# Kernel tuning notes

Measured on AMD Instinct MI355X. Metric: run time of the kernel, lower is better.

## Reference

```python
import jax, jax.numpy as jnp
import numpy as np
import math

N = 8192
H = 128
W = 128
TILE = 16
FOVX = math.pi / 3.0
FOVY = math.pi / 3.0
FOCAL_X = W / (2.0 * math.tan(FOVX * 0.5))
FOCAL_Y = H / (2.0 * math.tan(FOVY * 0.5))
WHITE_BKGD = True

# spherical-harmonic constants (degree 0..3), standard 3DGS eval_sh
C0 = 0.28209479177387814
C1 = 0.4886025119029199
C2 = (1.0925484305920792, -1.0925484305920792, 0.31539156525252005,
      -1.0925484305920792, 0.5462742152960396)
C3 = (-0.5900435899266435, 2.890611442640554, -0.4570457994644658,
      0.3731763325901154, -0.4570457994644658, 1.445305721320277,
      -0.5900435899266435)


def eval_sh3(sh, dirs):
    # sh: [N,3,16], dirs: [N,3] (unnormalized, as in the source)
    x, y, z = dirs[:, 0:1], dirs[:, 1:2], dirs[:, 2:3]
    res = C0 * sh[..., 0]
    res = res - C1 * y * sh[..., 1] + C1 * z * sh[..., 2] - C1 * x * sh[..., 3]
    xx, yy, zz = x * x, y * y, z * z
    xy, yz, xz = x * y, y * z, x * z
    res = (res + C2[0] * xy * sh[..., 4] + C2[1] * yz * sh[..., 5]
           + C2[2] * (2 * zz - xx - yy) * sh[..., 6]
           + C2[3] * xz * sh[..., 7] + C2[4] * (xx - yy) * sh[..., 8])
    res = (res + C3[0] * y * (3 * xx - yy) * sh[..., 9]
           + C3[1] * xy * z * sh[..., 10]
           + C3[2] * y * (4 * zz - xx - yy) * sh[..., 11]
           + C3[3] * z * (2 * zz - 3 * xx - 3 * yy) * sh[..., 12]
           + C3[4] * x * (4 * zz - xx - yy) * sh[..., 13]
           + C3[5] * z * (xx - yy) * sh[..., 14]
           + C3[6] * x * (xx - 3 * yy) * sh[..., 15])
    return res  # [N,3]


def _forward(means3D, opacity, scales, rotations, shs, viewmatrix, projmatrix, camera_center):
    f32 = means3D.dtype
    # ---- projection_ndc (row-vector convention) ----
    pts_o = jnp.concatenate([means3D, jnp.ones_like(means3D[:, :1])], -1)  # [N,4]
    pts_h = pts_o @ viewmatrix @ projmatrix
    p_proj = pts_h / (pts_h[:, -1:] + 1e-6)
    p_view = pts_o @ viewmatrix
    depths = p_view[:, 2]  # all points pass in_mask (z>=0.2) by construction

    # ---- build_color: SH degree 3 ----
    rays_d = means3D - camera_center
    color = jnp.maximum(eval_sh3(jnp.swapaxes(shs, 1, 2), rays_d) + 0.5, 0.0)  # [N,3]

    # ---- build_covariance_3d: L = R(q) @ diag(s); cov3d = L L^T ----
    q = rotations / jnp.linalg.norm(rotations, axis=1, keepdims=True)
    r, x, y, z = q[:, 0], q[:, 1], q[:, 2], q[:, 3]
    R = jnp.stack([1 - 2 * (y * y + z * z), 2 * (x * y - r * z), 2 * (x * z + r * y),
                   2 * (x * y + r * z), 1 - 2 * (x * x + z * z), 2 * (y * z - r * x),
                   2 * (x * z - r * y), 2 * (y * z + r * x), 1 - 2 * (x * x + y * y)],
                  axis=1).reshape(-1, 3, 3)
    L = R * scales[:, None, :]  # right-multiply by diag(s)
    cov3d = jnp.einsum('nij,nkj->nik', L, L)

    # ---- build_covariance_2d ----
    tanx, tany = math.tan(FOVX * 0.5), math.tan(FOVY * 0.5)
    t = means3D @ viewmatrix[:3, :3] + viewmatrix[3:4, :3]
    tz = t[:, 2]
    tx = jnp.clip(t[:, 0] / tz, -1.3 * tanx, 1.3 * tanx) * tz
    ty = jnp.clip(t[:, 1] / tz, -1.3 * tany, 1.3 * tany) * tz
    zr = jnp.zeros_like(tz)
    J = jnp.stack([FOCAL_X / tz, zr, -tx * FOCAL_X / (tz * tz),
                   zr, FOCAL_Y / tz, -ty * FOCAL_Y / (tz * tz),
                   zr, zr, zr], axis=1).reshape(-1, 3, 3)
    Wm = viewmatrix[:3, :3].T
    M = jnp.einsum('ij,njk,lk->nil', Wm, cov3d, Wm)
    cov2d = jnp.einsum('nab,nbc,ndc->nad', J, M, J)[:, :2, :2] + 0.3 * jnp.eye(2, dtype=f32)

    means2D = jnp.stack([((p_proj[:, 0] + 1) * W - 1.0) * 0.5,
                         ((p_proj[:, 1] + 1) * H - 1.0) * 0.5], -1)  # [N,2]

    # ---- radii / rect (computed under no_grad in the source) ----
    c2 = jax.lax.stop_gradient(cov2d)
    m2_ng = jax.lax.stop_gradient(means2D)
    det_ng = c2[:, 0, 0] * c2[:, 1, 1] - c2[:, 0, 1] * c2[:, 1, 0]
    mid = 0.5 * (c2[:, 0, 0] + c2[:, 1, 1])
    sq = jnp.sqrt(jnp.maximum(mid * mid - det_ng, 0.1))
    lam1 = mid + sq
    lam2 = mid - sq
    radii = 3.0 * jnp.ceil(jnp.sqrt(jnp.maximum(lam1, lam2)))
    rmin = m2_ng - radii[:, None]
    rmax = m2_ng + radii[:, None]
    rmin = jnp.stack([jnp.clip(rmin[:, 0], 0.0, W - 1.0), jnp.clip(rmin[:, 1], 0.0, H - 1.0)], -1)
    rmax = jnp.stack([jnp.clip(rmax[:, 0], 0.0, W - 1.0), jnp.clip(rmax[:, 1], 0.0, H - 1.0)], -1)

    # ---- global front-to-back depth sort (per-tile sort of a depth-sorted
    # subset equals the global sort restricted to that subset) ----
    order = jnp.argsort(depths)
    m2d_s = means2D[order]
    cov_s = cov2d[order]
    dep_s = depths[order]
    op_s = opacity[order, 0]  # [N]
    col_s = color[order]
    rmin_s = rmin[order]
    rmax_s = rmax[order]

    # analytic 2x2 inverse (conic)
    a, b = cov_s[:, 0, 0], cov_s[:, 0, 1]
    c, d = cov_s[:, 1, 0], cov_s[:, 1, 1]
    idet = 1.0 / (a * d - b * c)
    c00, c11 = d * idet, a * idet
    c01, c10 = -b * idet, -c * idet
    cxy = c01 + c10

    ty_n, tx_n = H // TILE, W // TILE

    def render_tile(tid):
        h = (tid // tx_n) * TILE
        w = (tid % tx_n) * TILE
        px = w + jnp.arange(TILE)
        py = h + jnp.arange(TILE)
        gx, gy = jnp.meshgrid(px, py)  # 'xy': gx[i,j]=px[j], gy[i,j]=py[i]
        coord = jnp.stack([gx, gy], -1).reshape(-1, 2).astype(f32)  # [P,2]=(x,y)
        # tile overlap test (replaces the data-dependent boolean gather)
        tlx = jnp.maximum(rmin_s[:, 0], w)
        tly = jnp.maximum(rmin_s[:, 1], h)
        brx = jnp.minimum(rmax_s[:, 0], w + TILE - 1)
        bry = jnp.minimum(rmax_s[:, 1], h + TILE - 1)
        in_mask = (brx > tlx) & (bry > tly)  # [N]
        dx = coord[:, None, :] - m2d_s[None]  # [P,N,2]
        power = -0.5 * (dx[..., 0] ** 2 * c00 + dx[..., 1] ** 2 * c11
                        + dx[..., 0] * dx[..., 1] * cxy)
        alpha = jnp.minimum(jnp.exp(power) * op_s[None, :], 0.99)
        alpha = alpha * in_mask[None, :].astype(f32)  # excluded gaussians contribute nothing
        T = jnp.cumprod(jnp.concatenate([jnp.ones_like(alpha[:, :1]),
                                         1.0 - alpha[:, :-1]], axis=1), axis=1)
        wgt = alpha * T  # [P,N]
        acc = jnp.sum(wgt, axis=1, keepdims=True)  # [P,1]
        bg = 1.0 if WHITE_BKGD else 0.0
        col = wgt @ col_s + (1.0 - acc) * bg  # [P,3]
        dep = wgt @ dep_s[:, None]  # [P,1]
        return (col.reshape(TILE, TILE, 3),
                dep.reshape(TILE, TILE, 1),
                acc.reshape(TILE, TILE, 1))

    cols, deps, accs = jax.lax.map(jax.checkpoint(render_tile), jnp.arange(ty_n * tx_n))

    def untile(xt):
        ch = xt.shape[-1]
        return xt.reshape(ty_n, tx_n, TILE, TILE, ch).transpose(0, 2, 1, 3, 4).reshape(H, W, ch)

    return untile(cols), untile(deps), untile(accs)


def setup_inputs() -> dict:
    key = jax.random.key(0)
    ks = jax.random.split(key, 6)
    xy = jax.random.uniform(ks[0], (N, 2), minval=-1.5, maxval=1.5)
    z = jax.random.uniform(ks[1], (N, 1), minval=2.0, maxval=6.0)  # all z>=0.2 -> in_mask all true
    means3D = jnp.concatenate([xy, z], -1)
    opacity = jax.random.uniform(ks[2], (N, 1), minval=0.1, maxval=1.0)
    scales = jax.random.uniform(ks[3], (N, 3), minval=0.01, maxval=0.08)
    rotations = jax.random.normal(ks[4], (N, 4))
    shs = jax.random.normal(ks[5], (N, 16, 3)) * 0.3
    viewmatrix = jnp.eye(4, dtype=jnp.float32)
    znear, zfar = 0.01, 100.0
    tfx, tfy = math.tan(FOVX * 0.5), math.tan(FOVY * 0.5)
    projmatrix = jnp.array([[1.0 / tfx, 0.0, 0.0, 0.0],
                            [0.0, 1.0 / tfy, 0.0, 0.0],
                            [0.0, 0.0, zfar / (zfar - znear), 1.0],
                            [0.0, 0.0, -(zfar * znear) / (zfar - znear), 0.0]],
                           dtype=jnp.float32)
    camera_center = jnp.zeros(3, dtype=jnp.float32)
    return {"means3D": means3D, "opacity": opacity, "scales": scales,
            "rotations": rotations, "shs": shs, "viewmatrix": viewmatrix,
            "projmatrix": projmatrix, "camera_center": camera_center}


def reference(means3D, opacity, scales, rotations, shs, viewmatrix, projmatrix, camera_center):
    return _forward(means3D, opacity, scales, rotations, shs,
                    viewmatrix, projmatrix, camera_center)
```

## Files before the change

### kernel.cpp

```cpp
#include <hip/hip_runtime.h>
#include <hip/hip_fp16.h>
#include <math.h>


#define NSLICE 16
#define CAP 192
#define CAP2 12
#define PRE_TPB 128
#define NPRE 64
#define TPB 256
#define NCELL (64 * NSLICE)

__global__ __launch_bounds__(PRE_TPB) void gs_preprocess(
    const float* __restrict__ means3D, const float* __restrict__ opacity,
    const float* __restrict__ scales, const float* __restrict__ rotations,
    const float* __restrict__ shs, const float* __restrict__ viewmatrix,
    const float* __restrict__ projmatrix, const float* __restrict__ camcenter,
    float4* __restrict__ A, float4* __restrict__ Bp,
    unsigned long long* __restrict__ list2, int* __restrict__ cnt2, int N)
{
    __shared__ int lcnt[NCELL];
    const int tid = threadIdx.x;
    const int blk = blockIdx.x;

    for (int k = tid; k < NCELL; k += PRE_TPB) lcnt[k] = 0;
    __syncthreads();

    const int i = blk * PRE_TPB + tid;
    if (i < N) {
        float V[16], P[16];
#pragma unroll
        for (int k = 0; k < 16; ++k) V[k] = viewmatrix[k];
#pragma unroll
        for (int k = 0; k < 16; ++k) P[k] = projmatrix[k];

        float mx = means3D[3*i+0], my = means3D[3*i+1], mz = means3D[3*i+2];

        float pv0 = mx*V[0] + my*V[4] + mz*V[8]  + V[12];
        float pv1 = mx*V[1] + my*V[5] + mz*V[9]  + V[13];
        float pv2 = mx*V[2] + my*V[6] + mz*V[10] + V[14];
        float pv3 = mx*V[3] + my*V[7] + mz*V[11] + V[15];

        float ph0 = pv0*P[0] + pv1*P[4] + pv2*P[8]  + pv3*P[12];
        float ph1 = pv0*P[1] + pv1*P[5] + pv2*P[9]  + pv3*P[13];
        float ph3 = pv0*P[3] + pv1*P[7] + pv2*P[11] + pv3*P[15];
        float invw = __builtin_amdgcn_rcpf(ph3 + 1e-6f);
        float ppx = ph0 * invw, ppy = ph1 * invw;
        float depth = pv2;

        float sh[48];
        {
            const float4* s4 = (const float4*)(shs + (size_t)i*48);
#pragma unroll
            for (int k = 0; k < 12; ++k) {
                float4 v4 = s4[k];
                sh[4*k+0] = v4.x; sh[4*k+1] = v4.y; sh[4*k+2] = v4.z; sh[4*k+3] = v4.w;
            }
        }
        float rdx = mx - camcenter[0], rdy = my - camcenter[1], rdz = mz - camcenter[2];
        float xx = rdx*rdx, yy = rdy*rdy, zz = rdz*rdz;
        float xy = rdx*rdy, yz = rdy*rdz, xz = rdx*rdz;
        const float C0 = 0.28209479177387814f;
        const float C1 = 0.4886025119029199f;
        const float C2_0 =  1.0925484305920792f, C2_1 = -1.0925484305920792f,
                    C2_2 =  0.31539156525252005f, C2_3 = -1.0925484305920792f,
                    C2_4 =  0.5462742152960396f;
        const float C3_0 = -0.5900435899266435f, C3_1 = 2.890611442640554f,
                    C3_2 = -0.4570457994644658f, C3_3 = 0.3731763325901154f,
                    C3_4 = -0.4570457994644658f, C3_5 = 1.445305721320277f,
                    C3_6 = -0.5900435899266435f;
        float col[3];
#pragma unroll
        for (int c = 0; c < 3; ++c) {
            float res = C0*sh[c]
                - C1*rdy*sh[3+c] + C1*rdz*sh[6+c] - C1*rdx*sh[9+c]
                + C2_0*xy*sh[12+c] + C2_1*yz*sh[15+c] + C2_2*(2.f*zz-xx-yy)*sh[18+c]
                + C2_3*xz*sh[21+c] + C2_4*(xx-yy)*sh[24+c]
                + C3_0*rdy*(3.f*xx-yy)*sh[27+c] + C3_1*xy*rdz*sh[30+c]
                + C3_2*rdy*(4.f*zz-xx-yy)*sh[33+c] + C3_3*rdz*(2.f*zz-3.f*xx-3.f*yy)*sh[36+c]
                + C3_4*rdx*(4.f*zz-xx-yy)*sh[39+c] + C3_5*rdz*(xx-yy)*sh[42+c]
                + C3_6*rdx*(xx-3.f*yy)*sh[45+c];
            col[c] = fmaxf(res + 0.5f, 0.0f);
        }

        float qr = rotations[4*i+0], qx = rotations[4*i+1], qy = rotations[4*i+2], qz = rotations[4*i+3];
        float qinv = __builtin_amdgcn_rsqf(qr*qr + qx*qx + qy*qy + qz*qz);
        qr *= qinv; qx *= qinv; qy *= qinv; qz *= qinv;
        float R00 = 1.f - 2.f*(qy*qy + qz*qz), R01 = 2.f*(qx*qy - qr*qz), R02 = 2.f*(qx*qz + qr*qy);
        float R10 = 2.f*(qx*qy + qr*qz), R11 = 1.f - 2.f*(qx*qx + qz*qz), R12 = 2.f*(qy*qz - qr*qx);
        float R20 = 2.f*(qx*qz - qr*qy), R21 = 2.f*(qy*qz + qr*qx), R22 = 1.f - 2.f*(qx*qx + qy*qy);
        float s0 = scales[3*i+0], s1 = scales[3*i+1], s2 = scales[3*i+2];
        float L00=R00*s0, L01=R01*s1, L02=R02*s2;
        float L10=R10*s0, L11=R11*s1, L12=R12*s2;
        float L20=R20*s0, L21=R21*s1, L22=R22*s2;
        float c300=L00*L00+L01*L01+L02*L02;
        float c301=L00*L10+L01*L11+L02*L12;
        float c302=L00*L20+L01*L21+L02*L22;
        float c311=L10*L10+L11*L11+L12*L12;
        float c312=L10*L20+L11*L21+L12*L22;
        float c322=L20*L20+L21*L21+L22*L22;

        const float TANX = 0.5773502691896257f;
        const float FX = 128.0f / (2.0f * TANX);
        float tz = pv2;
        float tzinv = __builtin_amdgcn_rcpf(tz);
        float limx = 1.3f * TANX;
        float txv = fminf(fmaxf(pv0 * tzinv, -limx), limx) * tz;
        float tyv = fminf(fmaxf(pv1 * tzinv, -limx), limx) * tz;
        float j00 = FX * tzinv, j02 = -txv * FX * tzinv * tzinv;
        float j11 = FX * tzinv, j12 = -tyv * FX * tzinv * tzinv;

        float Wm00=V[0], Wm01=V[4], Wm02=V[8];
        float Wm10=V[1], Wm11=V[5], Wm12=V[9];
        float Wm20=V[2], Wm21=V[6], Wm22=V[10];

        float t00 = Wm00*c300 + Wm01*c301 + Wm02*c302;
        float t01 = Wm00*c301 + Wm01*c311 + Wm02*c312;
        float t02 = Wm00*c302 + Wm01*c312 + Wm02*c322;
        float t10 = Wm10*c300 + Wm11*c301 + Wm12*c302;
        float t11 = Wm10*c301 + Wm11*c311 + Wm12*c312;
        float t12 = Wm10*c302 + Wm11*c312 + Wm12*c322;
        float t20 = Wm20*c300 + Wm21*c301 + Wm22*c302;
        float t21 = Wm20*c301 + Wm21*c311 + Wm22*c312;
        float t22 = Wm20*c302 + Wm21*c312 + Wm22*c322;
        float M00 = t00*Wm00 + t01*Wm01 + t02*Wm02;
        float M01 = t00*Wm10 + t01*Wm11 + t02*Wm12;
        float M02 = t00*Wm20 + t01*Wm21 + t02*Wm22;
        float M11 = t10*Wm10 + t11*Wm11 + t12*Wm12;
        float M12 = t10*Wm20 + t11*Wm21 + t12*Wm22;
        float M21 = t20*Wm10 + t21*Wm11 + t22*Wm12;
        float M20 = t20*Wm00 + t21*Wm01 + t22*Wm02;
        float M22 = t20*Wm20 + t21*Wm21 + t22*Wm22;

        float JM00 = j00*M00 + j02*M20;
        float JM01 = j00*M01 + j02*M21;
        float JM02 = j00*M02 + j02*M22;
        float JM11 = j11*M11 + j12*M21;
        float JM12 = j11*M12 + j12*M22;
        float a = JM00*j00 + JM02*j02 + 0.3f;
        float b = JM01*j11 + JM02*j12;
        float d = JM11*j11 + JM12*j12 + 0.3f;

        float m2x = ((ppx + 1.0f)*128.0f - 1.0f)*0.5f;
        float m2y = ((ppy + 1.0f)*128.0f - 1.0f)*0.5f;

        float det = a*d - b*b;
        float mid = 0.5f*(a + d);
        float sq = sqrtf(fmaxf(mid*mid - det, 0.1f));
        float radii = 3.0f * ceilf(sqrtf(fmaxf(mid + sq, mid - sq)));
        float rminx = fminf(fmaxf(m2x - radii, 0.0f), 127.0f);
        float rminy = fminf(fmaxf(m2y - radii, 0.0f), 127.0f);
        float rmaxx = fminf(fmaxf(m2x + radii, 0.0f), 127.0f);
        float rmaxy = fminf(fmaxf(m2y + radii, 0.0f), 127.0f);

        float idet = __builtin_amdgcn_rcpf(det);
        float c00i = d*idet, c11i = a*idet, cxyi = -2.0f*b*idet;

        unsigned colmask = 0, rowmask = 0;
#pragma unroll
        for (int c = 0; c < 8; ++c) {
            float wc = 16.0f * c;
            if (fminf(rmaxx, wc + 15.0f) > fmaxf(rminx, wc)) colmask |= 1u << c;
            if (fminf(rmaxy, wc + 15.0f) > fmaxf(rminy, wc)) rowmask |= 1u << c;
        }
        unsigned long long mask = 0;
#pragma unroll
        for (int r = 0; r < 8; ++r)
            if ((rowmask >> r) & 1) mask |= ((unsigned long long)colmask) << (8*r);

        unsigned kb = __float_as_uint(depth);
        kb = (kb & 0x80000000u) ? ~kb : (kb | 0x80000000u);

        unsigned rg = ((unsigned)__half_as_ushort(__float2half(col[1])) << 16)
                    |  (unsigned)__half_as_ushort(__float2half(col[0]));
        unsigned bd = ((unsigned)__half_as_ushort(__float2half(depth)) << 16)
                    |  (unsigned)__half_as_ushort(__float2half(col[2]));

        A[i]  = make_float4(m2x, m2y, c00i, c11i);
        Bp[i] = make_float4(cxyi, opacity[i], __uint_as_float(rg), __uint_as_float(bd));

        int sg = (int)((depth - 2.0f) * ((float)NSLICE / 4.0f));
        sg = sg < 0 ? 0 : (sg > NSLICE-1 ? NSLICE-1 : sg);

        unsigned long long key = (((unsigned long long)kb) << 32) | (unsigned)i;
        unsigned long long m = mask;
        while (m) {
            int t = __builtin_ctzll(m);
            m &= m - 1;
            int cell = t * NSLICE + sg;
            int pos = atomicAdd(&lcnt[cell], 1);
            if (pos < CAP2)
                list2[((size_t)cell * NPRE + blk) * CAP2 + pos] = key;
        }
    }
    __syncthreads();
    for (int k = tid; k < NCELL; k += PRE_TPB) {
        int c = lcnt[k];
        cnt2[(size_t)k * NPRE + blk] = c < CAP2 ? c : CAP2;
    }
}

__global__ __launch_bounds__(TPB) void gs_render(
    const float4* __restrict__ A, const float4* __restrict__ Bp,
    const unsigned long long* __restrict__ list2, const int* __restrict__ cnt2,
    float4* __restrict__ P1, float2* __restrict__ P2)
{
    __shared__ unsigned long long s_keys[CAP];
    __shared__ int s_sidx[CAP];
    __shared__ float4 sA[CAP], sBp[CAP];
    __shared__ int s_base[NPRE], s_cnt[NPRE];
    __shared__ int s_n;

    const int tid = threadIdx.x;
    const int slice = blockIdx.x;
    const int tile = blockIdx.y;
    const int h = (tile >> 3) * 16;
    const int w = (tile & 7) * 16;
    const int cell = tile * NSLICE + slice;

    if (tid < NPRE) {
        int c = cnt2[(size_t)cell * NPRE + tid];
        s_cnt[tid] = c;
        int pre = c;
#pragma unroll
        for (int s = 1; s < 64; s <<= 1) {
            int t = __shfl_up(pre, s);
            if (tid >= s) pre += t;
        }
        s_base[tid] = pre - c;
        if (tid == NPRE - 1) s_n = pre < CAP ? pre : CAP;
    }
    __syncthreads();
    const int n = s_n;

    {
        const int sub = tid & 63;
        const int c = s_cnt[sub];
        const int base = s_base[sub];
#pragma unroll
        for (int j = tid >> 6; j < CAP2; j += 4) {
            if (j < c) {
                int dst = base + j;
                if (dst < CAP)
                    s_keys[dst] = list2[((size_t)cell * NPRE + sub) * CAP2 + j];
            }
        }
    }
    __syncthreads();

    if (tid < n) {
        unsigned long long my = s_keys[tid];
        int r = 0;
        for (int j = 0; j < n; ++j) r += (s_keys[j] < my);
        s_sidx[r] = (int)(my & 0xffffffffu);
    }
    __syncthreads();

    if (tid < n) {
        int g = s_sidx[tid];
        sA[tid] = A[g]; sBp[tid] = Bp[g];
    }
    __syncthreads();

    const int pxi = tid & 15, pyi = tid >> 4;
    const float px = (float)(w + pxi), py = (float)(h + pyi);
    float T = 1.0f, acR = 0.f, acG = 0.f, acB = 0.f, acD = 0.f, acA = 0.f;

    for (int jj = 0; jj < n; ++jj) {
        float4 a4 = sA[jj];
        float4 bp = sBp[jj];
        float ddx = px - a4.x, ddy = py - a4.y;
        float power = -0.5f * (ddx*ddx*a4.z + ddy*ddy*a4.w + ddx*ddy*bp.x);
        unsigned rg = __float_as_uint(bp.z), bd = __float_as_uint(bp.w);
        float c_r = __half2float(__ushort_as_half((unsigned short)(rg & 0xffff)));
        float c_g = __half2float(__ushort_as_half((unsigned short)(rg >> 16)));
        float c_b = __half2float(__ushort_as_half((unsigned short)(bd & 0xffff)));
        float dpv = __half2float(__ushort_as_half((unsigned short)(bd >> 16)));
        float alpha = fminf(__expf(power) * bp.y, 0.99f);
        float wgt = alpha * T;
        acR += wgt * c_r; acG += wgt * c_g; acB += wgt * c_b;
        acD += wgt * dpv; acA += wgt;
        T *= (1.0f - alpha);
    }

    const int idx = (slice * 64 + tile) * TPB + tid;
    P1[idx] = make_float4(acR, acG, acB, acD);
    P2[idx] = make_float2(acA, T);
}

__global__ __launch_bounds__(TPB) void gs_combine(
    const float4* __restrict__ P1, const float2* __restrict__ P2,
    float* __restrict__ out)
{
    const int tid = threadIdx.x;
    const int tile = blockIdx.x;
    const int h = (tile >> 3) * 16;
    const int w = (tile & 7) * 16;

    float Tpre = 1.0f, cr = 0.f, cg = 0.f, cb = 0.f, dp = 0.f, ac = 0.f;
#pragma unroll
    for (int s = 0; s < NSLICE; ++s) {
        const int idx = (s * 64 + tile) * TPB + tid;
        float4 p1 = P1[idx];
        float2 p2 = P2[idx];
        cr += Tpre * p1.x; cg += Tpre * p1.y; cb += Tpre * p1.z;
        dp += Tpre * p1.w; ac += Tpre * p2.x;
        Tpre *= p2.y;
    }

    cr += (1.0f - ac); cg += (1.0f - ac); cb += (1.0f - ac);

    const int pxi = tid & 15, pyi = tid >> 4;
    const int y = h + pyi, x = w + pxi;
    const int pix = y * 128 + x;
    out[pix*3 + 0] = cr;
    out[pix*3 + 1] = cg;
    out[pix*3 + 2] = cb;
    out[128*128*3 + pix] = dp;
    out[128*128*3 + 128*128 + pix] = ac;
}

extern "C" void kernel_launch(void* const* d_in, const int* in_sizes, int n_in,
                              void* d_out, int out_size, void* d_ws, size_t ws_size,
                              hipStream_t stream) {
    const float* means3D    = (const float*)d_in[0];
    const float* opacity    = (const float*)d_in[1];
    const float* scales     = (const float*)d_in[2];
    const float* rotations  = (const float*)d_in[3];
    const float* shs        = (const float*)d_in[4];
    const float* viewmatrix = (const float*)d_in[5];
    const float* projmatrix = (const float*)d_in[6];
    const float* camcenter  = (const float*)d_in[7];
    float* out = (float*)d_out;

    int N = in_sizes[0] / 3;
    int nblk = (N + PRE_TPB - 1) / PRE_TPB;

    char* p = (char*)d_ws;
    float4* A = (float4*)p;                  p += (size_t)N * sizeof(float4);
    float4* Bp = (float4*)p;                 p += (size_t)N * sizeof(float4);
    float4* P1 = (float4*)p;                 p += (size_t)NSLICE * 64 * TPB * sizeof(float4);
    float2* P2 = (float2*)p;                 p += (size_t)NSLICE * 64 * TPB * sizeof(float2);
    unsigned long long* list2 = (unsigned long long*)p;
                                             p += (size_t)NCELL * NPRE * CAP2 * sizeof(unsigned long long);
    int* cnt2 = (int*)p;                     p += (size_t)NCELL * NPRE * sizeof(int);

    gs_preprocess<<<nblk, PRE_TPB, 0, stream>>>(
        means3D, opacity, scales, rotations, shs, viewmatrix, projmatrix,
        camcenter, A, Bp, list2, cnt2, N);

    gs_render<<<dim3(NSLICE, 64), TPB, 0, stream>>>(
        A, Bp, list2, cnt2, P1, P2);

    gs_combine<<<64, TPB, 0, stream>>>(P1, P2, out);
}
```

Before: 28.03 us.

## Fuse combine into render via recomputed prefix transmittance and atomic accumulation

Removes the separate combine kernel and the partial-result buffers. Each depth-slice block recomputes the transmittance of all earlier slices for its tile and atomically adds its weighted contribution into the output, which the preprocess kernel now zeroes. Empty slices exit early. This saves a launch and the global round trip of the partials, but later slices redo the alpha evaluation of every earlier slice, which adds up to roughly 15x extra work on the last slice, plus float atomic contention and a nondeterministic summation order.

After: 100.9 us. 3.6x slower.

```diff
diff --git a/kernel.cpp b/kernel.cpp
--- a/kernel.cpp
+++ b/kernel.cpp
@@ -17,11 +17,18 @@
     const float* __restrict__ shs, const float* __restrict__ viewmatrix,
     const float* __restrict__ projmatrix, const float* __restrict__ camcenter,
     float4* __restrict__ A, float4* __restrict__ Bp,
-    unsigned long long* __restrict__ list2, int* __restrict__ cnt2, int N)
+    unsigned long long* __restrict__ list2, int* __restrict__ cnt2,
+    float* __restrict__ out, int out_size, int N)
 {
     __shared__ int lcnt[NCELL];
     const int tid = threadIdx.x;
     const int blk = blockIdx.x;
+
+    {
+        const int nthr = gridDim.x * PRE_TPB;
+        for (int k = blk * PRE_TPB + tid; k < out_size; k += nthr)
+            out[k] = 0.0f;
+    }
 
     for (int k = tid; k < NCELL; k += PRE_TPB) lcnt[k] = 0;
     __syncthreads();
@@ -200,10 +207,10 @@
     }
 }
 
-__global__ __launch_bounds__(TPB) void gs_render(
+__global__ __launch_bounds__(TPB) void gs_render_combine(
     const float4* __restrict__ A, const float4* __restrict__ Bp,
     const unsigned long long* __restrict__ list2, const int* __restrict__ cnt2,
-    float4* __restrict__ P1, float2* __restrict__ P2)
+    float* __restrict__ out)
 {
     __shared__ unsigned long long s_keys[CAP];
     __shared__ int s_sidx[CAP];
@@ -233,7 +240,9 @@
     __syncthreads();
     const int n = s_n;
 
-    {
+    if (n == 0 && slice != NSLICE - 1) return;
+
+    if (n > 0) {
         const int sub = tid & 63;
         const int c = s_cnt[sub];
         const int base = s_base[sub];
@@ -245,22 +254,20 @@
                     s_keys[dst] = list2[((size_t)cell * NPRE + sub) * CAP2 + j];
             }
         }
-    }
-    __syncthreads();
-
-    if (tid < n) {
-        unsigned long long my = s_keys[tid];
-        int r = 0;
-        for (int j = 0; j < n; ++j) r += (s_keys[j] < my);
-        s_sidx[r] = (int)(my & 0xffffffffu);
-    }
-    __syncthreads();
-
-    if (tid < n) {
-        int g = s_sidx[tid];
-        sA[tid] = A[g]; sBp[tid] = Bp[g];
-    }
-    __syncthreads();
+        __syncthreads();
+        if (tid < n) {
+            unsigned long long my = s_keys[tid];
+            int r = 0;
+            for (int j = 0; j < n; ++j) r += (s_keys[j] < my);
+            s_sidx[r] = (int)(my & 0xffffffffu);
+        }
+        __syncthreads();
+        if (tid < n) {
+            int g = s_sidx[tid];
+            sA[tid] = A[g]; sBp[tid] = Bp[g];
+        }
+        __syncthreads();
+    }
 
     const int pxi = tid & 15, pyi = tid >> 4;
     const float px = (float)(w + pxi), py = (float)(h + pyi);
@@ -283,41 +290,68 @@
         T *= (1.0f - alpha);
     }
 
-    const int idx = (slice * 64 + tile) * TPB + tid;
-    P1[idx] = make_float4(acR, acG, acB, acD);
-    P2[idx] = make_float2(acA, T);
-}
-
-__global__ __launch_bounds__(TPB) void gs_combine(
-    const float4* __restrict__ P1, const float2* __restrict__ P2,
-    float* __restrict__ out)
-{
-    const int tid = threadIdx.x;
-    const int tile = blockIdx.x;
-    const int h = (tile >> 3) * 16;
-    const int w = (tile & 7) * 16;
-
-    float Tpre = 1.0f, cr = 0.f, cg = 0.f, cb = 0.f, dp = 0.f, ac = 0.f;
-#pragma unroll
-    for (int s = 0; s < NSLICE; ++s) {
-        const int idx = (s * 64 + tile) * TPB + tid;
-        float4 p1 = P1[idx];
-        float2 p2 = P2[idx];
-        cr += Tpre * p1.x; cg += Tpre * p1.y; cb += Tpre * p1.z;
-        dp += Tpre * p1.w; ac += Tpre * p2.x;
-        Tpre *= p2.y;
-    }
-
-    cr += (1.0f - ac); cg += (1.0f - ac); cb += (1.0f - ac);
-
-    const int pxi = tid & 15, pyi = tid >> 4;
+    float W = 1.0f;
+    for (int t = 0; t < slice; ++t) {
+        const int cellT = tile * NSLICE + t;
+        __syncthreads();
+        if (tid < NPRE) {
+            int c = cnt2[(size_t)cellT * NPRE + tid];
+            s_cnt[tid] = c;
+            int pre = c;
+#pragma unroll
+            for (int s = 1; s < 64; s <<= 1) {
+                int u = __shfl_up(pre, s);
+                if (tid >= s) pre += u;
+            }
+            s_base[tid] = pre - c;
+            if (tid == NPRE - 1) s_n = pre < CAP ? pre : CAP;
+        }
+        __syncthreads();
+        const int nt = s_n;
+        if (nt == 0) continue;
+
+        {
+            const int sub = tid & 63;
+            const int c = s_cnt[sub];
+            const int base = s_base[sub];
+#pragma unroll
+            for (int j = tid >> 6; j < CAP2; j += 4) {
+                if (j < c) {
+                    int dst = base + j;
+                    if (dst < CAP) {
+                        int g = (int)(list2[((size_t)cellT * NPRE + sub) * CAP2 + j]
+                                      & 0xffffffffu);
+                        sA[dst] = A[g]; sBp[dst] = Bp[g];
+                    }
+                }
+            }
+        }
+        __syncthreads();
+        for (int jj = 0; jj < nt; ++jj) {
+            float4 a4 = sA[jj];
+            float4 bp = sBp[jj];
+            float ddx = px - a4.x, ddy = py - a4.y;
+            float power = -0.5f * (ddx*ddx*a4.z + ddy*ddy*a4.w + ddx*ddy*bp.x);
+            float alpha = fminf(__expf(power) * bp.y, 0.99f);
+            W *= (1.0f - alpha);
+        }
+    }
+
     const int y = h + pyi, x = w + pxi;
     const int pix = y * 128 + x;
-    out[pix*3 + 0] = cr;
-    out[pix*3 + 1] = cg;
-    out[pix*3 + 2] = cb;
-    out[128*128*3 + pix] = dp;
-    out[128*128*3 + 128*128 + pix] = ac;
+    if (n > 0) {
+        atomicAdd(&out[pix*3 + 0], W * acR);
+        atomicAdd(&out[pix*3 + 1], W * acG);
+        atomicAdd(&out[pix*3 + 2], W * acB);
+        atomicAdd(&out[128*128*3 + pix], W * acD);
+        atomicAdd(&out[128*128*3 + 128*128 + pix], W * acA);
+    }
+    if (slice == NSLICE - 1) {
+        float Wbg = W * T;
+        atomicAdd(&out[pix*3 + 0], Wbg);
+        atomicAdd(&out[pix*3 + 1], Wbg);
+        atomicAdd(&out[pix*3 + 2], Wbg);
+    }
 }
 
 extern "C" void kernel_launch(void* const* d_in, const int* in_sizes, int n_in,
@@ -339,18 +373,14 @@
     char* p = (char*)d_ws;
     float4* A = (float4*)p;                  p += (size_t)N * sizeof(float4);
     float4* Bp = (float4*)p;                 p += (size_t)N * sizeof(float4);
-    float4* P1 = (float4*)p;                 p += (size_t)NSLICE * 64 * TPB * sizeof(float4);
-    float2* P2 = (float2*)p;                 p += (size_t)NSLICE * 64 * TPB * sizeof(float2);
     unsigned long long* list2 = (unsigned long long*)p;
                                              p += (size_t)NCELL * NPRE * CAP2 * sizeof(unsigned long long);
     int* cnt2 = (int*)p;                     p += (size_t)NCELL * NPRE * sizeof(int);
 
     gs_preprocess<<<nblk, PRE_TPB, 0, stream>>>(
         means3D, opacity, scales, rotations, shs, viewmatrix, projmatrix,
-        camcenter, A, Bp, list2, cnt2, N);
-
-    gs_render<<<dim3(NSLICE, 64), TPB, 0, stream>>>(
-        A, Bp, list2, cnt2, P1, P2);
-
-    gs_combine<<<64, TPB, 0, stream>>>(P1, P2, out);
+        camcenter, A, Bp, list2, cnt2, out, out_size, N);
+
+    gs_render_combine<<<dim3(NSLICE, 64), TPB, 0, stream>>>(
+        A, Bp, list2, cnt2, out);
 }
```
